# Kernel tuning notes

Hardware: AMD Instinct MI355X
Metric: run time of the kernel (lower is better)

## Reference

```python
import jax, jax.numpy as jnp
import numpy as np


def setup_inputs() -> dict:
    key = jax.random.key(0)
    N, C, E, S = 200000, 128, 3200000, 5000
    k0, k1, k2 = jax.random.split(key, 3)
    x = jax.random.normal(k0, (N, C), dtype=jnp.float32)
    edge_index = jax.random.randint(k1, (2, E), 0, N, dtype=jnp.int32)
    starts = (jnp.arange(S, dtype=jnp.int32) * (N // S))  # sorted sentence start offsets
    node1_indices = starts
    node2_indices = starts + 1
    sent_indices = starts + 2
    W = jax.random.normal(k2, (C, 1), dtype=jnp.float32) * 0.1
    b = jnp.zeros((1,), dtype=jnp.float32)
    return dict(x=x, edge_index=edge_index, node1_indices=node1_indices,
                node2_indices=node2_indices, sent_indices=sent_indices,
                W=W, b=b, alpha=4)


def _gcn_score(x, edge_index, W, b):
    # PyG GCNConv: h = xW; add self-loops; sym-normalized aggregation; + bias
    N = x.shape[0]
    h = x @ W  # [N, 1]
    row, col = edge_index[0], edge_index[1]
    ones = jnp.ones(row.shape[0], dtype=x.dtype)
    deg = jax.ops.segment_sum(ones, col, num_segments=N) + 1.0  # self-loop included
    dis = jax.lax.rsqrt(deg)
    norm = dis[row] * dis[col]
    agg = jax.ops.segment_sum(h[row] * norm[:, None], col, num_segments=N)
    out = agg + h * (dis * dis)[:, None]  # self-loop term, norm = 1/deg
    return (out + b).squeeze(-1)  # [N]


def reference(x, edge_index, node1_indices, node2_indices, sent_indices, W, b, alpha):
    N = x.shape[0]
    S = node1_indices.shape[0]
    score = _gcn_score(x, edge_index, W, b)  # [N]

    # per-sentence segment ids: segment i = [node1_indices[i], node1_indices[i+1])
    seg = jnp.searchsorted(node1_indices, jnp.arange(N, dtype=node1_indices.dtype), side='right') - 1
    seg = jnp.clip(seg, 0, S - 1)

    # numerically-stable per-segment softmax of scores
    m = jax.ops.segment_max(score, seg, num_segments=S)
    e = jnp.exp(score - m[seg])
    Z = jax.ops.segment_sum(e, seg, num_segments=S)
    p = e / Z[seg]  # normalized scores per sentence

    # cutoff = max(p) - alpha * std(p) per sentence (population std, as np.std)
    cnt = jax.ops.segment_sum(jnp.ones(N, dtype=p.dtype), seg, num_segments=S)
    pmax = jax.ops.segment_max(p, seg, num_segments=S)
    mean = jax.ops.segment_sum(p, seg, num_segments=S) / cnt
    var = jax.ops.segment_sum(p * p, seg, num_segments=S) / cnt - mean * mean
    std = jnp.sqrt(jnp.maximum(var, 0.0))
    cutoff = pmax - jnp.float32(alpha) * std
    keep = p >= cutoff[seg]

    # union with node1/node2/sent special nodes (always kept)
    keep = keep.at[node1_indices].set(True)
    keep = keep.at[node2_indices].set(True)
    keep = keep.at[sent_indices].set(True)

    # remap: position of each kept node in the compacted ordering
    pos = jnp.cumsum(keep.astype(jnp.int32)) - 1  # valid only where keep

    # gated node features (masked-dense form of x[perm] * tanh(score[perm]))
    x_out = jnp.where(keep[:, None], x * jnp.tanh(score)[:, None], 0.0)

    new_node1 = pos[node1_indices]
    new_node2 = pos[node2_indices]
    new_sent = pos[sent_indices]

    # filter_adj: keep edges with both endpoints kept, remap endpoints
    row, col = edge_index[0], edge_index[1]
    edge_keep = keep[row] & keep[col]
    new_edge_index = jnp.where(edge_keep[None, :], pos[edge_index], -1)

    return (x_out, new_edge_index, keep, edge_keep, new_node1, new_node2, new_sent)
```

## Files before the change

kernel.cpp:

```cpp
#include <hip/hip_runtime.h>
#include <math.h>

#define FXSCALE 4398046511104.0
#define WINDOW 7936
#define NBMAX 32
#define BINB 2048
#define SCAN_CHUNK 2048

typedef float vfloat4 __attribute__((ext_vector_type(4)));

__global__ void k_h_hist(const float* __restrict__ x, const float* __restrict__ W,
                         double* __restrict__ h,
                         const int* __restrict__ ecol, int* __restrict__ binCnt,
                         int N, int C, int E, int NB, int nhb) {
    int b = blockIdx.x;
    if (b < nhb) {
        int t = b * 256 + threadIdx.x;
        int row = t >> 5;
        int lane = t & 31;
        if (row >= N) return;
        const float4* xr = (const float4*)(x + (size_t)row * C);
        const float4* w4 = (const float4*)W;
        int C4 = C >> 2;
        double acc = 0.0;
        for (int c = lane; c < C4; c += 32) {
            float4 xv = xr[c];
            float4 wv = w4[c];
            acc += (double)xv.x * (double)wv.x + (double)xv.y * (double)wv.y
                 + (double)xv.z * (double)wv.z + (double)xv.w * (double)wv.w;
        }
        #pragma unroll
        for (int o = 16; o > 0; o >>= 1) acc += __shfl_xor(acc, o);
        if (lane == 0) h[row] = acc;
    } else {
        __shared__ int cnt[NBMAX];
        int tid = threadIdx.x;
        if (tid < NBMAX) cnt[tid] = 0;
        __syncthreads();
        int hb = b - nhb;
        for (long e = (long)hb * 256 + tid; e < E; e += 512L * 256)
            atomicAdd(&cnt[ecol[e] / WINDOW], 1);
        __syncthreads();
        if (tid < NB && cnt[tid] > 0) atomicAdd(&binCnt[tid], cnt[tid]);
    }
}

__global__ void k_off(const int* __restrict__ binCnt, int* __restrict__ binOff,
                      int* __restrict__ binWr, int NB) {
    if (threadIdx.x != 0 || blockIdx.x != 0) return;
    int acc = 0;
    for (int i = 0; i < NB; i++) {
        binOff[i] = acc;
        binWr[i] = acc;
        acc += binCnt[i];
    }
    binOff[NB] = acc;
}

__global__ void k_bin(const int* __restrict__ erow, const int* __restrict__ ecol,
                      int* __restrict__ binWr, int* __restrict__ binnedRow,
                      unsigned short* __restrict__ binnedCol16, int E, int NB) {
    __shared__ int cnt[NBMAX];
    __shared__ int lbase[NBMAX];
    __shared__ int gbase[NBMAX];
    __shared__ int lrow[BINB];
    __shared__ unsigned short lcol[BINB];
    __shared__ unsigned char lbin[BINB];
    int tid = threadIdx.x;
    if (tid < NBMAX) cnt[tid] = 0;
    __syncthreads();
    long b0 = (long)blockIdx.x * BINB;
    int n = (int)((E - b0) < (long)BINB ? (E - b0) : (long)BINB);
    int bA[8], rkA[8], rwA[8];
    unsigned short clA[8];
    #pragma unroll
    for (int k = 0; k < 8; k++) bA[k] = -1;
    int base_i = tid * 8;
    if (base_i + 8 <= n) {
        long e = b0 + base_i;
        int4 r0 = *(const int4*)(erow + e), r1 = *(const int4*)(erow + e + 4);
        int4 c0 = *(const int4*)(ecol + e), c1 = *(const int4*)(ecol + e + 4);
        int rr[8] = {r0.x, r0.y, r0.z, r0.w, r1.x, r1.y, r1.z, r1.w};
        int cc[8] = {c0.x, c0.y, c0.z, c0.w, c1.x, c1.y, c1.z, c1.w};
        #pragma unroll
        for (int k = 0; k < 8; k++) {
            int c = cc[k];
            int bb = c / WINDOW;
            bA[k] = bb; rwA[k] = rr[k]; clA[k] = (unsigned short)(c - bb * WINDOW);
            rkA[k] = atomicAdd(&cnt[bb], 1);
        }
    } else {
        for (int k = 0; k < 8; k++) {
            int i = base_i + k;
            if (i < n) {
                long e = b0 + i;
                int c = ecol[e];
                int bb = c / WINDOW;
                bA[k] = bb; rwA[k] = erow[e]; clA[k] = (unsigned short)(c - bb * WINDOW);
                rkA[k] = atomicAdd(&cnt[bb], 1);
            }
        }
    }
    __syncthreads();
    if (tid == 0) {
        int acc = 0;
        for (int i = 0; i < NB; i++) { lbase[i] = acc; acc += cnt[i]; }
    }
    __syncthreads();
    if (tid < NB && cnt[tid] > 0) gbase[tid] = atomicAdd(&binWr[tid], cnt[tid]);
    __syncthreads();
    #pragma unroll
    for (int k = 0; k < 8; k++) {
        if (bA[k] >= 0) {
            int l = lbase[bA[k]] + rkA[k];
            lrow[l] = rwA[k];
            lcol[l] = clA[k];
            lbin[l] = (unsigned char)bA[k];
        }
    }
    __syncthreads();
    for (int l = tid; l < n; l += 256) {
        int bb = lbin[l];
        int g = gbase[bb] + (l - lbase[bb]);
        binnedRow[g] = lrow[l];
        binnedCol16[g] = lcol[l];
    }
}

__global__ void k_degb(const unsigned short* __restrict__ binnedCol16,
                       const int* __restrict__ binOff,
                       unsigned int* __restrict__ partialDeg, int N, int Md) {
    __shared__ unsigned int cnt[WINDOW];
    int bin = blockIdx.x / Md, m = blockIdx.x % Md;
    int tid = threadIdx.x;
    for (int i = tid; i < WINDOW; i += blockDim.x) cnt[i] = 0;
    __syncthreads();
    int st = binOff[bin], en = binOff[bin + 1];
    for (int idx = st + m * (int)blockDim.x + tid; idx < en; idx += Md * (int)blockDim.x)
        atomicAdd(&cnt[binnedCol16[idx]], 1u);
    __syncthreads();
    int wb = bin * WINDOW;
    for (int i = tid; i < WINDOW && wb + i < N; i += blockDim.x)
        partialDeg[(size_t)m * N + wb + i] = cnt[i];
}

__global__ void k_dis_hd(const unsigned int* __restrict__ partialDeg,
                         const double* __restrict__ h,
                         double* __restrict__ dis, double* __restrict__ hd,
                         int N, int Md) {
    int i = blockIdx.x * blockDim.x + threadIdx.x;
    if (i >= N) return;
    unsigned int dsum = 0;
    for (int m = 0; m < Md; m++) dsum += partialDeg[(size_t)m * N + i];
    double d = 1.0 / sqrt((double)dsum + 1.0);
    dis[i] = d;
    hd[i] = h[i] * d;
}

__global__ void k_aggb(const int* __restrict__ binnedRow,
                       const unsigned short* __restrict__ binnedCol16,
                       const int* __restrict__ binOff,
                       const double* __restrict__ hd, const double* __restrict__ dis,
                       unsigned long long* __restrict__ partialAgg, int N, int Ma) {
    __shared__ unsigned long long acc[WINDOW];
    int bin = blockIdx.x / Ma, m = blockIdx.x % Ma;
    int tid = threadIdx.x;
    for (int i = tid; i < WINDOW; i += blockDim.x) acc[i] = 0ULL;
    __syncthreads();
    int st = binOff[bin], en = binOff[bin + 1];
    int wb = bin * WINDOW;
    for (int idx = st + m * (int)blockDim.x + tid; idx < en; idx += Ma * (int)blockDim.x) {
        int r = binnedRow[idx];
        int c16 = binnedCol16[idx];
        long long q = __double2ll_rn(hd[r] * dis[wb + c16] * FXSCALE);
        atomicAdd(&acc[c16], (unsigned long long)q);
    }
    __syncthreads();
    for (int i = tid; i < WINDOW && wb + i < N; i += blockDim.x)
        partialAgg[(size_t)m * N + wb + i] = acc[i];
}

__global__ void k_score(const unsigned long long* __restrict__ partialAgg,
                        const double* __restrict__ h, const double* __restrict__ dis,
                        const float* __restrict__ bptr,
                        float* __restrict__ score32, float* __restrict__ tg,
                        int N, int Ma) {
    int i = blockIdx.x * blockDim.x + threadIdx.x;
    if (i >= N) return;
    long long acc = 0;
    for (int m = 0; m < Ma; m++) acc += (long long)partialAgg[(size_t)m * N + i];
    double agg = (double)acc / FXSCALE;
    double d = dis[i];
    double sc = (agg + h[i] * (d * d)) + (double)bptr[0];
    score32[i] = (float)sc;
    tg[i] = (float)tanh(sc);
}

__global__ void k_seg_np(const float* __restrict__ score32, const int* __restrict__ starts,
                         float* __restrict__ p32, int* __restrict__ keepI,
                         const int* __restrict__ alphaPtr,
                         const int* __restrict__ n1, const int* __restrict__ n2,
                         const int* __restrict__ sent, int N, int S) {
    int g = blockIdx.x * blockDim.x + threadIdx.x;
    if (g >= S) return;
    int st = starts[g];
    int en = (g == S - 1) ? N : starts[g + 1];
    if (en <= st) return;

    int ai = alphaPtr[0];
    float alpha = (ai >= 0 && ai < 1000000) ? (float)ai : __int_as_float(ai);

    float m = -3.402823466e38f;
    for (int i = st; i < en; i++) m = fmaxf(m, score32[i]);

    float Z = 0.0f;
    for (int i = st; i < en; i++) {
        float dm = __fsub_rn(score32[i], m);
        float e = (float)exp((double)dm);
        p32[i] = e;
        Z = __fadd_rn(Z, e);
    }

    float sp = 0.0f, sq = 0.0f, pm = -3.402823466e38f;
    for (int i = st; i < en; i++) {
        float p = __fdiv_rn(p32[i], Z);
        p32[i] = p;
        sp = __fadd_rn(sp, p);
        sq = __fadd_rn(sq, __fmul_rn(p, p));
        pm = fmaxf(pm, p);
    }

    float cnt_ = (float)(en - st);
    float mean = __fdiv_rn(sp, cnt_);
    float var = __fsub_rn(__fdiv_rn(sq, cnt_), __fmul_rn(mean, mean));
    float sd = sqrtf(fmaxf(var, 0.0f));
    float cutoff = __fsub_rn(pm, __fmul_rn(alpha, sd));

    for (int i = st; i < en; i++) keepI[i] = (p32[i] >= cutoff) ? 1 : 0;

    keepI[n1[g]] = 1;
    keepI[n2[g]] = 1;
    keepI[sent[g]] = 1;
}

__global__ void k_scan(const int* __restrict__ keepI, const float* __restrict__ tg,
                       unsigned long long* __restrict__ stArr,
                       float* __restrict__ posF, float* __restrict__ gate,
                       float* __restrict__ o_keep, int N) {
    int tid = threadIdx.x;
    int b = blockIdx.x;
    long base = (long)b * SCAN_CHUNK + (long)tid * 8;
    int v[8];
    int th = 0;
    #pragma unroll
    for (int k = 0; k < 8; k++) {
        long i = base + k;
        v[k] = (i < N) ? keepI[i] : 0;
        th += v[k];
    }
    __shared__ int sm[256];
    sm[tid] = th; __syncthreads();
    for (int off = 1; off < 256; off <<= 1) {
        int t = (tid >= off) ? sm[tid - off] : 0;
        __syncthreads();
        sm[tid] += t;
        __syncthreads();
    }
    int total = sm[255];
    __shared__ int exclSh;
    if (tid == 0) {
        if (b == 0) {
            atomicExch(&stArr[0], (2ULL << 62) | (unsigned long long)(unsigned)total);
            exclSh = 0;
        } else {
            atomicExch(&stArr[b], (1ULL << 62) | (unsigned long long)(unsigned)total);
            int excl = 0;
            int j = b - 1;
            while (true) {
                unsigned long long s = atomicAdd(&stArr[j], 0ULL);
                unsigned state = (unsigned)(s >> 62);
                if (state == 0) continue;
                excl += (int)(s & 0x3FFFFFFFFFFFFFFFULL);
                if (state == 2u) break;
                j--;
            }
            atomicExch(&stArr[b], (2ULL << 62) | (unsigned long long)(unsigned)(excl + total));
            exclSh = excl;
        }
    }
    __syncthreads();
    int run = exclSh + sm[tid] - th;
    #pragma unroll
    for (int k = 0; k < 8; k++) {
        long i = base + k;
        if (i < N) {
            posF[i] = v[k] ? (float)(run + v[k] - 1) : -1.0f;
            gate[i] = v[k] ? tg[i] : 0.0f;
            o_keep[i] = v[k] ? 1.0f : 0.0f;
            run += v[k];
        }
    }
}

__global__ void k_out(const float4* __restrict__ x4, const float* __restrict__ gate,
                      float* __restrict__ o_x, long total4,
                      const int* __restrict__ erow, const int* __restrict__ ecol,
                      const float* __restrict__ posF,
                      float* __restrict__ o_edge, float* __restrict__ o_ekeep, int E,
                      const int* __restrict__ n1, const int* __restrict__ n2,
                      const int* __restrict__ sent,
                      float* __restrict__ o_n1, float* __restrict__ o_n2,
                      float* __restrict__ o_sent, int S,
                      int nxb, int neb4) {
    int b = blockIdx.x;
    if (b < nxb) {
        long idx = (long)b * blockDim.x + threadIdx.x;
        if (idx >= total4) return;
        int row = (int)(idx >> 5);
        float g = gate[row];
        float4 v = x4[idx];
        vfloat4 r = { v.x * g, v.y * g, v.z * g, v.w * g };
        __builtin_nontemporal_store(r, (vfloat4*)o_x + idx);
    } else if (b < nxb + neb4) {
        long e0 = ((long)(b - nxb) * blockDim.x + threadIdx.x) * 4;
        if (e0 >= E) return;
        if (e0 + 3 < E) {
            int4 r4 = *(const int4*)(erow + e0);
            int4 c4 = *(const int4*)(ecol + e0);
            vfloat4 oer, oec, ok;
            #pragma unroll
            for (int k = 0; k < 4; k++) {
                int r = (&r4.x)[k], c = (&c4.x)[k];
                float pr = posF[r], pc = posF[c];
                bool ek = (pr >= 0.0f) && (pc >= 0.0f);
                oer[k] = ek ? pr : -1.0f;
                oec[k] = ek ? pc : -1.0f;
                ok[k]  = ek ? 1.0f : 0.0f;
            }
            __builtin_nontemporal_store(oer, (vfloat4*)(o_edge + e0));
            __builtin_nontemporal_store(oec, (vfloat4*)(o_edge + (size_t)E + e0));
            __builtin_nontemporal_store(ok,  (vfloat4*)(o_ekeep + e0));
        } else {
            for (long e = e0; e < E; e++) {
                int r = erow[e], c = ecol[e];
                float pr = posF[r], pc = posF[c];
                bool ek = (pr >= 0.0f) && (pc >= 0.0f);
                o_edge[e] = ek ? pr : -1.0f;
                o_edge[(size_t)E + e] = ek ? pc : -1.0f;
                o_ekeep[e] = ek ? 1.0f : 0.0f;
            }
        }
    } else {
        int i = (b - nxb - neb4) * blockDim.x + threadIdx.x;
        if (i >= S) return;
        o_n1[i] = posF[n1[i]];
        o_n2[i] = posF[n2[i]];
        o_sent[i] = posF[sent[i]];
    }
}

extern "C" void kernel_launch(void* const* d_in, const int* in_sizes, int n_in,
                              void* d_out, int out_size, void* d_ws, size_t ws_size,
                              hipStream_t stream) {
    const float* x    = (const float*)d_in[0];
    const int*   eidx = (const int*)d_in[1];
    const int*   n1   = (const int*)d_in[2];
    const int*   n2   = (const int*)d_in[3];
    const int*   sent = (const int*)d_in[4];
    const float* W    = (const float*)d_in[5];
    const float* bp   = (const float*)d_in[6];
    const int*   alphaPtr = (const int*)d_in[7];

    int C = in_sizes[5];
    int N = in_sizes[0] / C;
    int E = in_sizes[1] / 2;
    int S = in_sizes[2];

    const int* erow = eidx;
    const int* ecol = eidx + E;

    int NB = (N + WINDOW - 1) / WINDOW;
    const int Md = 8, Ma = 8;

    char* ws = (char*)d_ws;
    size_t off = 0;
    auto alloc = [&](size_t bytes) { void* p = ws + off; off += (bytes + 255) & ~(size_t)255; return p; };
    int*   binCnt = (int*)  alloc(NBMAX * 4);
    unsigned long long* scanSt = (unsigned long long*)alloc(256 * 8);
    size_t zeroBytes = (size_t)((char*)(scanSt + 256) - (char*)binCnt);
    int*   binOff = (int*)  alloc((NBMAX + 1) * 4);
    int*   binWr  = (int*)  alloc(NBMAX * 4);
    int*   binnedRow = (int*)alloc((size_t)E * 4);
    unsigned short* binnedCol16 = (unsigned short*)alloc((size_t)E * 2);
    unsigned int* partialDeg = (unsigned int*)alloc((size_t)Md * N * 4);
    unsigned long long* partialAgg = (unsigned long long*)alloc((size_t)Ma * N * 8);
    double* h     = (double*)alloc((size_t)N * 8);
    double* dis   = (double*)alloc((size_t)N * 8);
    double* hd    = (double*)alloc((size_t)N * 8);
    float* score32 = (float*)alloc((size_t)N * 4);
    float* p32    = (float*)alloc((size_t)N * 4);
    float* tg     = (float*)alloc((size_t)N * 4);
    int*   keepI  = (int*)  alloc((size_t)N * 4);
    float* posF   = (float*)alloc((size_t)N * 4);
    float* gate   = (float*)alloc((size_t)N * 4);

    float* o_x     = (float*)d_out;
    float* o_edge  = o_x + (size_t)N * C;
    float* o_keep  = o_edge + 2 * (size_t)E;
    float* o_ekeep = o_keep + N;
    float* o_n1    = o_ekeep + E;
    float* o_n2    = o_n1 + S;
    float* o_sent  = o_n2 + S;

    (void)hipMemsetAsync(binCnt, 0, zeroBytes, stream);

    int nhb = (N * 32 + 255) / 256;
    k_h_hist<<<nhb + 512, 256, 0, stream>>>(x, W, h, ecol, binCnt, N, C, E, NB, nhb);
    k_off<<<1, 64, 0, stream>>>(binCnt, binOff, binWr, NB);
    int nBatches = (int)(((long)E + BINB - 1) / BINB);
    k_bin<<<nBatches, 256, 0, stream>>>(erow, ecol, binWr, binnedRow, binnedCol16, E, NB);
    k_degb<<<NB * Md, 256, 0, stream>>>(binnedCol16, binOff, partialDeg, N, Md);
    k_dis_hd<<<(N + 255) / 256, 256, 0, stream>>>(partialDeg, h, dis, hd, N, Md);
    k_aggb<<<NB * Ma, 256, 0, stream>>>(binnedRow, binnedCol16, binOff, hd, dis, partialAgg, N, Ma);
    k_score<<<(N + 255) / 256, 256, 0, stream>>>(partialAgg, h, dis, bp, score32, tg, N, Ma);
    k_seg_np<<<(S + 255) / 256, 256, 0, stream>>>(score32, n1, p32, keepI, alphaPtr, n1, n2, sent, N, S);
    int nb = (N + SCAN_CHUNK - 1) / SCAN_CHUNK;
    k_scan<<<nb, 256, 0, stream>>>(keepI, tg, scanSt, posF, gate, o_keep, N);

    long total4 = (long)N * (C / 4);
    int nxb = (int)((total4 + 255) / 256);
    long e4 = (E + 3) / 4;
    int neb4 = (int)((e4 + 255) / 256);
    int nsb = (S + 255) / 256;
    k_out<<<nxb + neb4 + nsb, 256, 0, stream>>>(
        (const float4*)x, gate, o_x, total4,
        erow, ecol, posF, o_edge, o_ekeep, E,
        n1, n2, sent, o_n1, o_n2, o_sent, S, nxb, neb4);
}
```

Before: 252.4 us.

## Shrink bin window, drop offset kernel, fuse h-matvec into binning launch

Cuts the column window from 7936 to 1984, giving about 101 bins instead of 26, so the degree and aggregation kernels launch roughly four times as many blocks with smaller shared-memory footprints. The single-thread offset kernel is removed; each binning, degree and aggregation block now derives its bin offset by summing earlier bin counts itself. The x·W matvec moves from the histogram launch into the binning launch, and the histogram becomes its own kernel. The changes target launch count and low occupancy in the per-bin kernels, at the cost of redundant prefix sums and more scatter targets during binning.

```diff
diff --git a/kernel.cpp b/kernel.cpp
--- a/kernel.cpp
+++ b/kernel.cpp
@@ -2,20 +2,36 @@
 #include <math.h>
 
 #define FXSCALE 4398046511104.0
-#define WINDOW 7936
-#define NBMAX 32
+#define WINDOW 1984
+#define NBMAX 128
 #define BINB 2048
 #define SCAN_CHUNK 2048
 
 typedef float vfloat4 __attribute__((ext_vector_type(4)));
 
-__global__ void k_h_hist(const float* __restrict__ x, const float* __restrict__ W,
-                         double* __restrict__ h,
-                         const int* __restrict__ ecol, int* __restrict__ binCnt,
-                         int N, int C, int E, int NB, int nhb) {
-    int b = blockIdx.x;
-    if (b < nhb) {
-        int t = b * 256 + threadIdx.x;
+__global__ void k_hist(const int* __restrict__ ecol, int* __restrict__ binCnt,
+                       int E, int NB) {
+    __shared__ int cnt[NBMAX];
+    int tid = threadIdx.x;
+    for (int i = tid; i < NBMAX; i += 256) cnt[i] = 0;
+    __syncthreads();
+    for (long e = (long)blockIdx.x * 256 + tid; e < E; e += 512L * 256)
+        atomicAdd(&cnt[ecol[e] / WINDOW], 1);
+    __syncthreads();
+    for (int i = tid; i < NB; i += 256)
+        if (cnt[i] > 0) atomicAdd(&binCnt[i], cnt[i]);
+}
+
+__global__ void k_bin_h(const int* __restrict__ erow, const int* __restrict__ ecol,
+                        const int* __restrict__ binCnt, int* __restrict__ binWr0,
+                        int* __restrict__ binnedRow,
+                        unsigned short* __restrict__ binnedCol16,
+                        const float* __restrict__ x, const float* __restrict__ W,
+                        double* __restrict__ h,
+                        int E, int NB, int N, int C, int nBatches) {
+    int blk = blockIdx.x;
+    if (blk >= nBatches) {
+        int t = (blk - nBatches) * 256 + threadIdx.x;
         int row = t >> 5;
         int lane = t & 31;
         if (row >= N) return;
@@ -32,34 +48,8 @@
         #pragma unroll
         for (int o = 16; o > 0; o >>= 1) acc += __shfl_xor(acc, o);
         if (lane == 0) h[row] = acc;
-    } else {
-        __shared__ int cnt[NBMAX];
-        int tid = threadIdx.x;
-        if (tid < NBMAX) cnt[tid] = 0;
-        __syncthreads();
-        int hb = b - nhb;
-        for (long e = (long)hb * 256 + tid; e < E; e += 512L * 256)
-            atomicAdd(&cnt[ecol[e] / WINDOW], 1);
-        __syncthreads();
-        if (tid < NB && cnt[tid] > 0) atomicAdd(&binCnt[tid], cnt[tid]);
-    }
-}
-
-__global__ void k_off(const int* __restrict__ binCnt, int* __restrict__ binOff,
-                      int* __restrict__ binWr, int NB) {
-    if (threadIdx.x != 0 || blockIdx.x != 0) return;
-    int acc = 0;
-    for (int i = 0; i < NB; i++) {
-        binOff[i] = acc;
-        binWr[i] = acc;
-        acc += binCnt[i];
-    }
-    binOff[NB] = acc;
-}
-
-__global__ void k_bin(const int* __restrict__ erow, const int* __restrict__ ecol,
-                      int* __restrict__ binWr, int* __restrict__ binnedRow,
-                      unsigned short* __restrict__ binnedCol16, int E, int NB) {
+        return;
+    }
     __shared__ int cnt[NBMAX];
     __shared__ int lbase[NBMAX];
     __shared__ int gbase[NBMAX];
@@ -67,9 +57,9 @@
     __shared__ unsigned short lcol[BINB];
     __shared__ unsigned char lbin[BINB];
     int tid = threadIdx.x;
-    if (tid < NBMAX) cnt[tid] = 0;
-    __syncthreads();
-    long b0 = (long)blockIdx.x * BINB;
+    for (int i = tid; i < NBMAX; i += 256) cnt[i] = 0;
+    __syncthreads();
+    long b0 = (long)blk * BINB;
     int n = (int)((E - b0) < (long)BINB ? (E - b0) : (long)BINB);
     int bA[8], rkA[8], rwA[8];
     unsigned short clA[8];
@@ -104,10 +94,15 @@
     __syncthreads();
     if (tid == 0) {
         int acc = 0;
+        #pragma unroll 1
         for (int i = 0; i < NB; i++) { lbase[i] = acc; acc += cnt[i]; }
     }
     __syncthreads();
-    if (tid < NB && cnt[tid] > 0) gbase[tid] = atomicAdd(&binWr[tid], cnt[tid]);
+    if (tid < NB && cnt[tid] > 0) {
+        int boff = 0;
+        for (int i = 0; i < tid; i++) boff += binCnt[i];
+        gbase[tid] = boff + atomicAdd(&binWr0[tid], cnt[tid]);
+    }
     __syncthreads();
     #pragma unroll
     for (int k = 0; k < 8; k++) {
@@ -128,19 +123,27 @@
 }
 
 __global__ void k_degb(const unsigned short* __restrict__ binnedCol16,
-                       const int* __restrict__ binOff,
-                       unsigned int* __restrict__ partialDeg, int N, int Md) {
+                       const int* __restrict__ binCnt,
+                       unsigned int* __restrict__ partialDeg, int N, int Md, int NB) {
     __shared__ unsigned int cnt[WINDOW];
+    __shared__ int boff[2];
     int bin = blockIdx.x / Md, m = blockIdx.x % Md;
     int tid = threadIdx.x;
-    for (int i = tid; i < WINDOW; i += blockDim.x) cnt[i] = 0;
-    __syncthreads();
-    int st = binOff[bin], en = binOff[bin + 1];
-    for (int idx = st + m * (int)blockDim.x + tid; idx < en; idx += Md * (int)blockDim.x)
+    if (tid == 0) {
+        int acc = 0;
+        for (int i = 0; i < bin; i++) acc += binCnt[i];
+        boff[0] = acc;
+        boff[1] = acc + binCnt[bin];
+    }
+    for (int i = tid; i < WINDOW; i += 256) cnt[i] = 0;
+    __syncthreads();
+    int st = boff[0], en = boff[1];
+    for (int idx = st + m * 256 + tid; idx < en; idx += Md * 256)
         atomicAdd(&cnt[binnedCol16[idx]], 1u);
     __syncthreads();
     int wb = bin * WINDOW;
-    for (int i = tid; i < WINDOW && wb + i < N; i += blockDim.x)
+    int wlim = (N - wb) < WINDOW ? (N - wb) : WINDOW;
+    for (int i = tid; i < wlim; i += 256)
         partialDeg[(size_t)m * N + wb + i] = cnt[i];
 }
 
@@ -159,24 +162,32 @@
 
 __global__ void k_aggb(const int* __restrict__ binnedRow,
                        const unsigned short* __restrict__ binnedCol16,
-                       const int* __restrict__ binOff,
+                       const int* __restrict__ binCnt,
                        const double* __restrict__ hd, const double* __restrict__ dis,
-                       unsigned long long* __restrict__ partialAgg, int N, int Ma) {
+                       unsigned long long* __restrict__ partialAgg, int N, int Ma, int NB) {
     __shared__ unsigned long long acc[WINDOW];
+    __shared__ int boff[2];
     int bin = blockIdx.x / Ma, m = blockIdx.x % Ma;
     int tid = threadIdx.x;
-    for (int i = tid; i < WINDOW; i += blockDim.x) acc[i] = 0ULL;
-    __syncthreads();
-    int st = binOff[bin], en = binOff[bin + 1];
+    if (tid == 0) {
+        int a = 0;
+        for (int i = 0; i < bin; i++) a += binCnt[i];
+        boff[0] = a;
+        boff[1] = a + binCnt[bin];
+    }
+    for (int i = tid; i < WINDOW; i += 256) acc[i] = 0ULL;
+    __syncthreads();
+    int st = boff[0], en = boff[1];
     int wb = bin * WINDOW;
-    for (int idx = st + m * (int)blockDim.x + tid; idx < en; idx += Ma * (int)blockDim.x) {
+    for (int idx = st + m * 256 + tid; idx < en; idx += Ma * 256) {
         int r = binnedRow[idx];
         int c16 = binnedCol16[idx];
         long long q = __double2ll_rn(hd[r] * dis[wb + c16] * FXSCALE);
         atomicAdd(&acc[c16], (unsigned long long)q);
     }
     __syncthreads();
-    for (int i = tid; i < WINDOW && wb + i < N; i += blockDim.x)
+    int wlim = (N - wb) < WINDOW ? (N - wb) : WINDOW;
+    for (int i = tid; i < wlim; i += 256)
         partialAgg[(size_t)m * N + wb + i] = acc[i];
 }
 
@@ -386,10 +397,9 @@
     size_t off = 0;
     auto alloc = [&](size_t bytes) { void* p = ws + off; off += (bytes + 255) & ~(size_t)255; return p; };
     int*   binCnt = (int*)  alloc(NBMAX * 4);
+    int*   binWr0 = (int*)  alloc(NBMAX * 4);
     unsigned long long* scanSt = (unsigned long long*)alloc(256 * 8);
     size_t zeroBytes = (size_t)((char*)(scanSt + 256) - (char*)binCnt);
-    int*   binOff = (int*)  alloc((NBMAX + 1) * 4);
-    int*   binWr  = (int*)  alloc(NBMAX * 4);
     int*   binnedRow = (int*)alloc((size_t)E * 4);
     unsigned short* binnedCol16 = (unsigned short*)alloc((size_t)E * 2);
     unsigned int* partialDeg = (unsigned int*)alloc((size_t)Md * N * 4);
@@ -414,14 +424,15 @@
 
     (void)hipMemsetAsync(binCnt, 0, zeroBytes, stream);
 
+    k_hist<<<512, 256, 0, stream>>>(ecol, binCnt, E, NB);
+    int nBatches = (int)(((long)E + BINB - 1) / BINB);
     int nhb = (N * 32 + 255) / 256;
-    k_h_hist<<<nhb + 512, 256, 0, stream>>>(x, W, h, ecol, binCnt, N, C, E, NB, nhb);
-    k_off<<<1, 64, 0, stream>>>(binCnt, binOff, binWr, NB);
-    int nBatches = (int)(((long)E + BINB - 1) / BINB);
-    k_bin<<<nBatches, 256, 0, stream>>>(erow, ecol, binWr, binnedRow, binnedCol16, E, NB);
-    k_degb<<<NB * Md, 256, 0, stream>>>(binnedCol16, binOff, partialDeg, N, Md);
+    k_bin_h<<<nBatches + nhb, 256, 0, stream>>>(erow, ecol, binCnt, binWr0,
+                                                binnedRow, binnedCol16,
+                                                x, W, h, E, NB, N, C, nBatches);
+    k_degb<<<NB * Md, 256, 0, stream>>>(binnedCol16, binCnt, partialDeg, N, Md, NB);
     k_dis_hd<<<(N + 255) / 256, 256, 0, stream>>>(partialDeg, h, dis, hd, N, Md);
-    k_aggb<<<NB * Ma, 256, 0, stream>>>(binnedRow, binnedCol16, binOff, hd, dis, partialAgg, N, Ma);
+    k_aggb<<<NB * Ma, 256, 0, stream>>>(binnedRow, binnedCol16, binCnt, hd, dis, partialAgg, N, Ma, NB);
     k_score<<<(N + 255) / 256, 256, 0, stream>>>(partialAgg, h, dis, bp, score32, tg, N, Ma);
     k_seg_np<<<(S + 255) / 256, 256, 0, stream>>>(score32, n1, p32, keepI, alphaPtr, n1, n2, sent, N, S);
     int nb = (N + SCAN_CHUNK - 1) / SCAN_CHUNK;
```

New measurement: 251.7 us. About the same (-0.3%).
